# Kernel optimization log

Measured on AMD Instinct MI355X. Metric: run time of the kernel, lower is better.

## Reference

```python
import jax, jax.numpy as jnp
import numpy as np


def setup_inputs() -> dict:
    key = jax.random.key(0)
    ks = jax.random.split(key, 12)
    C, H, L, P = 256, 8, 4, 4
    Lq, Lx = 2048, 300
    iss = jnp.array([[64, 64], [32, 32], [16, 16], [8, 8]], dtype=jnp.int32)
    Len_in = int(np.sum(np.array(iss)[:, 0] * np.array(iss)[:, 1]))  # 5440
    lsi = jnp.array([0, 4096, 5120, 5376], dtype=jnp.int32)
    return {
        "query": jax.random.normal(ks[0], (1, Lq, C), jnp.float32),
        "reference_points": jax.random.uniform(ks[1], (1, Lq, L, 2), jnp.float32),
        "input_flatten": jax.random.normal(ks[2], (1, Len_in, C), jnp.float32),
        "input_spatial_shapes": iss,
        "add_keys": jax.random.normal(ks[3], (1, Lx, C), jnp.float32),
        "input_level_start_index": lsi,
        "W_off": jax.random.normal(ks[4], (H * L * P * 2, C), jnp.float32) * 0.01,
        "b_off": jax.random.normal(ks[5], (H * L * P * 2,), jnp.float32),
        "W_attn": jax.random.normal(ks[6], (H * (L + 1), C, C), jnp.float32) * 0.05,
        "W_v": jax.random.normal(ks[7], (H * 2, C, C), jnp.float32) * 0.05,
        "b_v": jax.random.normal(ks[8], (H * 2, C), jnp.float32) * 0.01,
        "W_mix": jax.random.normal(ks[9], (C, H + 1), jnp.float32) * 0.5,
    }


def reference(query, reference_points, input_flatten, input_spatial_shapes,
              add_keys, input_level_start_index, W_off, b_off, W_attn, W_v, b_v, W_mix):
    N, Lq, C = query.shape
    L = input_spatial_shapes.shape[0]
    H = W_v.shape[0] // 2
    P = W_off.shape[0] // (H * L * 2)

    # sampling locations: ref (x,y in [0,1]) + offsets / (W,H)
    off = (query @ W_off.T + b_off).reshape(N, Lq, H, L, P, 2)
    wh = input_spatial_shapes[:, ::-1].astype(query.dtype)  # (L,2) = (W,H)
    loc = reference_points[:, :, None, :, None, :] + off / wh[None, None, None, :, None, :]

    # get_keys: truncating index computation + gather (faithful to original)
    loc = jnp.clip(loc, 0.0, 0.999)
    iss_f = input_spatial_shapes.astype(loc.dtype)[None, None, None, :, None, :]
    idx = (loc * iss_f).astype(jnp.int32)  # (N,Lq,H,L,P,2): (int(x*H_l), int(y*W_l))
    lin = (idx[..., 0]
           + idx[..., 1] * input_spatial_shapes[:, 0].astype(jnp.int32)[None, None, None, :, None]
           + input_level_start_index.astype(jnp.int32)[None, None, None, :, None])
    keys = input_flatten[0][lin[0]]                # (Lq,H,L,P,C)
    keys = jnp.transpose(keys, (1, 2, 3, 0, 4))    # (H,L,P,Lq,C)

    head_w = jax.nn.softmax(W_mix.T, axis=0)       # (H+1,C)
    qf = query[0]                                  # (Lq,C)
    ak = add_keys[0]                               # (Lx,C)

    # per-head, per-level similarity (replicates original overlapping index h*L+lvl)
    Ws = W_attn[jnp.arange(H)[:, None] * L + jnp.arange(L)[None, :]]  # (H,L,C,C)
    T = jnp.einsum('hlce,hlpqe->hlcpq', Ws, keys)  # (H,L,C,P,Lq)
    # faithful reshape quirk: (C, P*Lq) viewed as (P, Lq, C)
    T = T.reshape(H, L, P, Lq, C)
    attn_s = jnp.einsum('hlpqc,qc->hlpq', T, qf).reshape(H, L * P, Lq)

    Wadd = W_attn[jnp.arange(H) * L + L]           # (H,C,C)
    attn_a = jnp.einsum('xe,hce,qc->hxq', ak, Wadd, qf)  # (H,Lx,Lq)

    attn = jax.nn.softmax(jnp.concatenate([attn_s, attn_a], axis=1), axis=1)
    attn_s_sm, attn_a_sm = attn[:, :L * P], attn[:, L * P:]

    Wv0, bv0 = W_v[0::2], b_v[0::2]
    Wv1, bv1 = W_v[1::2], b_v[1::2]
    vals = (jnp.einsum('hlpqe,hce->hlpqc', keys, Wv0)
            + bv0[:, None, None, None, :]).reshape(H, L * P, Lq, C)
    v2 = jnp.einsum('xe,hce->hxc', ak, Wv1) + bv1[:, None, :]  # (H,Lx,C)

    out_h = (jnp.einsum('hkq,hkqc->hqc', attn_s_sm, vals)
             + jnp.einsum('hxq,hxc->hqc', attn_a_sm, v2))      # (H,Lq,C)
    result = qf * head_w[-1][None, :] + jnp.einsum('hqc,hc->qc', out_h, head_w[:-1])
    return result[None]
```

## Files before the change

kernel.cpp:

```cpp
#include <hip/hip_runtime.h>
#include <stdint.h>

#define NJ 316

typedef __attribute__((ext_vector_type(8))) short short8;
typedef __attribute__((ext_vector_type(4))) float f32x4;
union U4S8 { uint4 u; short8 s; };

__device__ __forceinline__ unsigned short f2bf(float x) {
    unsigned int u = __float_as_uint(x);
    u += 0x7fff + ((u >> 16) & 1);
    return (unsigned short)(u >> 16);
}
__device__ __forceinline__ float bf2f(unsigned short h) {
    return __uint_as_float(((unsigned int)h) << 16);
}

__global__ __launch_bounds__(256) void cvt_all_kernel(
    const float* __restrict__ q,  unsigned short* __restrict__ qh,  unsigned short* __restrict__ ql,
    const float* __restrict__ ak, unsigned short* __restrict__ akh, unsigned short* __restrict__ akl,
    const float* __restrict__ wv, unsigned short* __restrict__ wvh, unsigned short* __restrict__ wvl,
    const float* __restrict__ inflat, unsigned int* __restrict__ inflatP,
    const float* __restrict__ Wattn, unsigned short* __restrict__ wah, unsigned short* __restrict__ wal,
    unsigned short* __restrict__ v2th, unsigned short* __restrict__ v2tl)
{
    int i = blockIdx.x * 256 + threadIdx.x;
    if (i < 760576) {
        const float* s; unsigned short *dh, *dl; int off; bool pack = false;
        unsigned int* dp = nullptr;
        if (i < 131072)      { s = q;  dh = qh;  dl = ql;  off = i; }
        else if (i < 150272) { s = ak; dh = akh; dl = akl; off = i - 131072; }
        else if (i < 412416) { s = wv; dh = wvh; dl = wvl; off = i - 150272; }
        else { s = inflat; dp = inflatP; off = i - 412416; pack = true; dh = dl = nullptr; }
        float4 v = ((const float4*)s)[off];
        float x[4] = {v.x, v.y, v.z, v.w};
        unsigned short h[4], l[4];
        #pragma unroll
        for (int j = 0; j < 4; ++j) {
            h[j] = f2bf(x[j]);
            l[j] = f2bf(x[j] - bf2f(h[j]));
        }
        if (pack) {
            ((uint4*)dp)[off] = make_uint4(
                (unsigned)h[0] | ((unsigned)l[0] << 16),
                (unsigned)h[1] | ((unsigned)l[1] << 16),
                (unsigned)h[2] | ((unsigned)l[2] << 16),
                (unsigned)h[3] | ((unsigned)l[3] << 16));
        } else {
            ((uint2*)dh)[off] = make_uint2((unsigned)h[0] | ((unsigned)h[1] << 16),
                                           (unsigned)h[2] | ((unsigned)h[3] << 16));
            ((uint2*)dl)[off] = make_uint2((unsigned)l[0] | ((unsigned)l[1] << 16),
                                           (unsigned)l[2] | ((unsigned)l[3] << 16));
        }
    } else if (i < 891648) {
        int off = i - 760576;
        int base = off * 4;
        int z = base >> 16, r = base & 65535;
        float4 v = *(const float4*)&Wattn[(size_t)(4 * z + 4) * 65536 + r];
        float x[4] = {v.x, v.y, v.z, v.w};
        unsigned short h[4], l[4];
        #pragma unroll
        for (int j = 0; j < 4; ++j) {
            h[j] = f2bf(x[j]);
            l[j] = f2bf(x[j] - bf2f(h[j]));
        }
        ((uint2*)wah)[off] = make_uint2((unsigned)h[0] | ((unsigned)h[1] << 16),
                                        (unsigned)h[2] | ((unsigned)h[3] << 16));
        ((uint2*)wal)[off] = make_uint2((unsigned)l[0] | ((unsigned)l[1] << 16),
                                        (unsigned)l[2] | ((unsigned)l[3] << 16));
    } else {
        int j = i - 891648;
        size_t base = (size_t)j * 320;
        uint2 zz = make_uint2(0u, 0u);
        #pragma unroll
        for (int d = 0; d < 4; ++d) {
            ((uint2*)(v2th + base))[d] = zz;
            ((uint2*)(v2tl + base))[d] = zz;
        }
        ((uint2*)(v2th + base + 316))[0] = zz;
        ((uint2*)(v2tl + base + 316))[0] = zz;
    }
}

struct Seg {
    const unsigned short *Ah, *Al, *Bh, *Bl;
    int K, lda, ldb;
    long sA, sB;
    int nprod;
};

template<bool ACCUM, bool OUTF32, int NSEG>
__device__ __forceinline__ void gemm_core(
    const Seg& s0, const Seg& s1,
    float* __restrict__ Cf, unsigned short* __restrict__ Ch,
    unsigned short* __restrict__ Cl,
    int M, int N, int ldc, long sC, int nb, int mb, int z, char* smem)
{
    unsigned short* As0 = (unsigned short*)smem;
    unsigned short* Bs0 = (unsigned short*)(smem + 10240);
    const int t = threadIdx.x;
    const int lane = t & 63;
    const int wave = t >> 6;
    const int wm = (wave & 1) * 32, wn = (wave >> 1) * 64;

    f32x4 acc[2][4];
    #pragma unroll
    for (int i = 0; i < 2; ++i)
        #pragma unroll
        for (int j = 0; j < 4; ++j) acc[i][j] = (f32x4){0.f, 0.f, 0.f, 0.f};

    const int arow = t >> 2, akoff = (t & 3) * 8;
    const int frow = lane & 15, fk = (lane >> 4) * 8;

    #pragma unroll
    for (int seg = 0; seg < NSEG; ++seg) {
        const Seg S = seg ? s1 : s0;
        const int np = S.nprod;
        const unsigned short* Azh = S.Ah + (size_t)z * S.sA;
        const unsigned short* Azl = (np >= 2) ? S.Al + (size_t)z * S.sA : nullptr;
        const unsigned short* Bzh = S.Bh + (size_t)z * S.sB;
        const unsigned short* Bzl = (np >= 3) ? S.Bl + (size_t)z * S.sB : nullptr;
        for (int kb = 0; kb < S.K; kb += 32) {
            __syncthreads();
            {
                int gm = mb + arow;
                uint4 vh = {0, 0, 0, 0}, vl = {0, 0, 0, 0};
                if (gm < M) {
                    size_t o = (size_t)gm * S.lda + kb + akoff;
                    vh = *(const uint4*)(Azh + o);
                    if (np >= 2) vl = *(const uint4*)(Azl + o);
                }
                *(uint4*)&As0[arow * 40 + akoff] = vh;
                if (np >= 2) *(uint4*)&As0[2560 + arow * 40 + akoff] = vl;
                #pragma unroll
                for (int i = 0; i < 2; ++i) {
                    int f = i * 256 + t;
                    int brow = f >> 2, bkoff = (f & 3) * 8;
                    int gn = nb + brow;
                    uint4 wh = {0, 0, 0, 0}, wl = {0, 0, 0, 0};
                    if (gn < N) {
                        size_t o = (size_t)gn * S.ldb + kb + bkoff;
                        wh = *(const uint4*)(Bzh + o);
                        if (np >= 3) wl = *(const uint4*)(Bzl + o);
                    }
                    *(uint4*)&Bs0[brow * 40 + bkoff] = wh;
                    if (np >= 3) *(uint4*)&Bs0[5120 + brow * 40 + bkoff] = wl;
                }
            }
            __syncthreads();
            short8 a[2][2], b[4][2];
            #pragma unroll
            for (int i = 0; i < 2; ++i) {
                int r = wm + i * 16 + frow;
                a[i][0] = *(const short8*)&As0[r * 40 + fk];
                if (np >= 2) a[i][1] = *(const short8*)&As0[2560 + r * 40 + fk];
            }
            #pragma unroll
            for (int j = 0; j < 4; ++j) {
                int r = wn + j * 16 + frow;
                b[j][0] = *(const short8*)&Bs0[r * 40 + fk];
                if (np >= 3) b[j][1] = *(const short8*)&Bs0[5120 + r * 40 + fk];
            }
            #pragma unroll
            for (int i = 0; i < 2; ++i)
                #pragma unroll
                for (int j = 0; j < 4; ++j) {
                    acc[i][j] = __builtin_amdgcn_mfma_f32_16x16x32_bf16(
                        a[i][0], b[j][0], acc[i][j], 0, 0, 0);
                    if (np >= 2)
                        acc[i][j] = __builtin_amdgcn_mfma_f32_16x16x32_bf16(
                            a[i][1], b[j][0], acc[i][j], 0, 0, 0);
                    if (np >= 3)
                        acc[i][j] = __builtin_amdgcn_mfma_f32_16x16x32_bf16(
                            a[i][0], b[j][1], acc[i][j], 0, 0, 0);
                }
        }
    }
    #pragma unroll
    for (int i = 0; i < 2; ++i)
        #pragma unroll
        for (int r = 0; r < 4; ++r) {
            int gm = mb + wm + i * 16 + (lane >> 4) * 4 + r;
            if (gm >= M) continue;
            #pragma unroll
            for (int j = 0; j < 4; ++j) {
                int gn = nb + wn + j * 16 + (lane & 15);
                if (gn >= N) continue;
                size_t idx = (size_t)z * sC + (size_t)gm * ldc + gn;
                float v = acc[i][j][r];
                if (OUTF32) {
                    float prev = ACCUM ? Cf[idx] : 0.f;
                    Cf[idx] = prev + v;
                } else {
                    unsigned short h = f2bf(v);
                    Ch[idx] = h;
                    Cl[idx] = f2bf(v - bf2f(h));
                }
            }
        }
}

template<bool ACCUM, bool OUTF32, int NSEG>
__global__ __launch_bounds__(256) void mfma_gemm(
    Seg s0, Seg s1,
    float* __restrict__ Cf, unsigned short* __restrict__ Ch,
    unsigned short* __restrict__ Cl,
    int M, int N, int ldc, long sC)
{
    __shared__ __align__(16) char smem[30720];
    gemm_core<ACCUM, OUTF32, NSEG>(s0, s1, Cf, Ch, Cl, M, N, ldc, sC,
                                   blockIdx.x * 128, blockIdx.y * 64,
                                   blockIdx.z, smem);
}

__global__ __launch_bounds__(256) void dual_lin_kernel(
    Seg a, Seg b,
    unsigned short* __restrict__ Bhh, unsigned short* __restrict__ Bhl,
    unsigned short* __restrict__ V2Th, unsigned short* __restrict__ V2Tl,
    const float* __restrict__ q, const float* __restrict__ refp,
    const int* __restrict__ iss, const int* __restrict__ lsi,
    const float* __restrict__ Woff, const float* __restrict__ boff,
    int* __restrict__ lin)
{
    __shared__ __align__(16) char smem[58368];
    const int bx = blockIdx.x;
    if (bx < 2) {
        gemm_core<false, false, 1>(a, a, nullptr, Bhh, Bhl,
                                   300, 256, 256, 320L * 256,
                                   bx * 128, blockIdx.y * 64, blockIdx.z, smem);
        return;
    }
    if (bx < 5) {
        if ((int)blockIdx.y * 64 >= 256) return;
        gemm_core<false, false, 1>(b, b, nullptr, V2Th, V2Tl,
                                   256, 300, 320, 256L * 320,
                                   (bx - 2) * 128, blockIdx.y * 64, blockIdx.z,
                                   smem);
        return;
    }
    const int idx = (bx - 5) * 40 + blockIdx.y * 8 + blockIdx.z;
    if (idx >= 256) return;

    float (*qf8)[256]  = (float(*)[256])smem;
    float (*wtile)[33] = (float(*)[33])(smem + 8192);
    double (*offl)[256]= (double(*)[256])(smem + 41984);
    const int t = threadIdx.x;
    const int qbase = idx * 8;
    #pragma unroll
    for (int i = 0; i < 8; ++i) qf8[i][t] = q[(qbase + i) * 256 + t];
    double acc[8];
    #pragma unroll
    for (int r = 0; r < 8; ++r) acc[r] = 0.0;
    for (int cb = 0; cb < 256; cb += 32) {
        __syncthreads();
        #pragma unroll
        for (int i = 0; i < 32; ++i) {
            int f = i * 256 + t;
            int o = f >> 5, jj = f & 31;
            wtile[o][jj] = Woff[o * 256 + cb + jj];
        }
        __syncthreads();
        #pragma unroll
        for (int jj = 0; jj < 32; ++jj) {
            double wvv = (double)wtile[t][jj];
            #pragma unroll
            for (int r = 0; r < 8; ++r)
                acc[r] += (double)qf8[r][cb + jj] * wvv;
        }
    }
    double bo = (double)boff[t];
    __syncthreads();
    #pragma unroll
    for (int r = 0; r < 8; ++r) offl[r][t] = acc[r] + bo;
    __syncthreads();
    #pragma unroll
    for (int rep = 0; rep < 4; ++rep) {
        int id2 = rep * 256 + t;
        int r = id2 >> 7;
        int s = id2 & 127;
        int l = (s >> 2) & 3;
        int qq = qbase + r;
        double offx = offl[r][2 * s];
        double offy = offl[r][2 * s + 1];
        int w0 = iss[l * 2 + 0];
        int w1 = iss[l * 2 + 1];
        double locx = (double)refp[qq * 8 + l * 2 + 0] + offx / (double)w1;
        double locy = (double)refp[qq * 8 + l * 2 + 1] + offy / (double)w0;
        locx = fmin(fmax(locx, 0.0), 0.999);
        locy = fmin(fmax(locy, 0.0), 0.999);
        int ix = (int)(locx * (double)w0);
        int iy = (int)(locy * (double)w1);
        lin[qq * 128 + s] = ix + iy * w0 + lsi[l];
    }
}

__global__ __launch_bounds__(256, 2) void gattn_attnA(
    const unsigned short* __restrict__ qh, const unsigned short* __restrict__ ql,
    const unsigned int* __restrict__ inflatP, const float* __restrict__ Wattn,
    const int* __restrict__ lin, float* __restrict__ attn, Seg aA)
{
    __shared__ __align__(16) char smem[69632];
    const int t = threadIdx.x;

    if ((int)blockIdx.x >= 1024) {
        int idx = blockIdx.x - 1024;
        int z = idx & 7, my = (idx >> 3) & 31, nx = idx >> 8;
        gemm_core<false, true, 1>(aA, aA, attn + 16, nullptr, nullptr,
                                  2048, 300, NJ, 2048L * NJ,
                                  nx * 128, my * 64, z, smem);
        return;
    }

    int* linrow = (int*)smem;
    float (*Glds)[268] = (float(*)[268])(smem + 1024);
    const int lane = t & 63, w = t >> 6;
    const int b = blockIdx.x;
    const int qb = b & 7, p = (b >> 3) & 3, l = (b >> 5) & 3, h = b >> 7;
    linrow[t] = lin[(256 * qb + t) * 128 + h * 16 + l * 4 + p];
    __syncthreads();

    const int l15 = lane & 15, g = lane >> 4;
    const int q2l = qb + 8 * p + 32 * l15;
    const int ebase = 64 * w + l15;

    f32x4 acc[4][4];
    #pragma unroll
    for (int i = 0; i < 4; ++i)
        #pragma unroll
        for (int eg = 0; eg < 4; ++eg) acc[i][eg] = (f32x4){0.f, 0.f, 0.f, 0.f};

    for (int kb = 0; kb < 256; kb += 32) {
        U4S8 ah[4], al[4];
        #pragma unroll
        for (int i = 0; i < 4; ++i) {
            size_t off = (size_t)(q2l + 512 * i) * 256 + kb + 8 * g;
            ah[i].u = *(const uint4*)(qh + off);
            al[i].u = *(const uint4*)(ql + off);
        }
        int rowoff[8];
        #pragma unroll
        for (int m = 0; m < 8; ++m) rowoff[m] = linrow[kb + 8 * g + m] * 256;
        unsigned int uv[4][8];
        #pragma unroll
        for (int eg = 0; eg < 4; ++eg)
            #pragma unroll
            for (int m = 0; m < 8; ++m)
                uv[eg][m] = inflatP[rowoff[m] + ebase + 16 * eg];

        #pragma unroll
        for (int eg = 0; eg < 4; ++eg) {
            U4S8 bh, bl;
            unsigned int hh[4], ll[4];
            #pragma unroll
            for (int d = 0; d < 4; ++d) {
                hh[d] = __builtin_amdgcn_perm(uv[eg][2 * d + 1], uv[eg][2 * d],
                                              0x05040100u);
                ll[d] = __builtin_amdgcn_perm(uv[eg][2 * d + 1], uv[eg][2 * d],
                                              0x07060302u);
            }
            bh.u = make_uint4(hh[0], hh[1], hh[2], hh[3]);
            bl.u = make_uint4(ll[0], ll[1], ll[2], ll[3]);
            #pragma unroll
            for (int i = 0; i < 4; ++i) {
                acc[i][eg] = __builtin_amdgcn_mfma_f32_16x16x32_bf16(
                    ah[i].s, bh.s, acc[i][eg], 0, 0, 0);
                acc[i][eg] = __builtin_amdgcn_mfma_f32_16x16x32_bf16(
                    ah[i].s, bl.s, acc[i][eg], 0, 0, 0);
                acc[i][eg] = __builtin_amdgcn_mfma_f32_16x16x32_bf16(
                    al[i].s, bh.s, acc[i][eg], 0, 0, 0);
            }
        }
    }

    #pragma unroll
    for (int i = 0; i < 4; ++i)
        #pragma unroll
        for (int eg = 0; eg < 4; ++eg)
            #pragma unroll
            for (int r = 0; r < 4; ++r)
                Glds[16 * i + 4 * g + r][64 * w + 16 * eg + l15] = acc[i][eg][r];
    __syncthreads();

    const int tx = t & 15, ty = t >> 4;
    const float* Wsbase = Wattn + (size_t)(h * 4 + l) * 65536;
    float gv[4][16];
    #pragma unroll
    for (int r = 0; r < 4; ++r)
        #pragma unroll
        for (int i2 = 0; i2 < 4; ++i2) {
            float4 gd = *(const float4*)&Glds[ty * 4 + r][tx * 4 + 64 * i2];
            gv[r][i2 * 4 + 0] = gd.x;
            gv[r][i2 * 4 + 1] = gd.y;
            gv[r][i2 * 4 + 2] = gd.z;
            gv[r][i2 * 4 + 3] = gd.w;
        }
    #pragma unroll
    for (int r = 0; r < 4; ++r) {
        int hi = ty * 4 + r;
        int q2 = qb + 8 * p + 32 * hi;
        #pragma unroll
        for (int p2 = 0; p2 < 4; ++p2) {
            const float* wr = Wsbase + (size_t)(hi + 64 * p2) * 256;
            float partial = 0.f;
            #pragma unroll
            for (int i2 = 0; i2 < 4; ++i2) {
                float4 wv = *(const float4*)&wr[tx * 4 + 64 * i2];
                partial += wv.x * gv[r][i2 * 4 + 0] + wv.y * gv[r][i2 * 4 + 1]
                         + wv.z * gv[r][i2 * 4 + 2] + wv.w * gv[r][i2 * 4 + 3];
            }
            partial += __shfl_xor(partial, 1);
            partial += __shfl_xor(partial, 2);
            partial += __shfl_xor(partial, 4);
            partial += __shfl_xor(partial, 8);
            if (tx == 0)
                attn[((size_t)h * 2048 + q2) * NJ + (l * 4 + p2)] = partial;
        }
    }
}

__global__ __launch_bounds__(256) void softmax_ka_kernel(
    const float* __restrict__ attn, const unsigned int* __restrict__ inflatP,
    const int* __restrict__ lin, float* __restrict__ s0,
    unsigned short* __restrict__ awh,
    unsigned short* __restrict__ KAh, unsigned short* __restrict__ KAl)
{
    __shared__ float red[8];
    __shared__ float w16[16];
    __shared__ int lls[16];
    const int t = threadIdx.x;
    const int lane = t & 63, w = t >> 6;
    const int rid = blockIdx.x;
    const int h = rid >> 11, q = rid & 2047;
    const float* row = attn + (size_t)rid * NJ;

    float v0 = row[t];
    float v1 = (t < 60) ? row[256 + t] : -1e30f;
    float m = fmaxf(v0, v1);
    #pragma unroll
    for (int d = 1; d < 64; d <<= 1) m = fmaxf(m, __shfl_xor(m, d));
    if (lane == 0) red[w] = m;
    __syncthreads();
    m = fmaxf(fmaxf(red[0], red[1]), fmaxf(red[2], red[3]));

    float e0 = expf(v0 - m);
    float e1 = (t < 60) ? expf(v1 - m) : 0.f;
    float s = e0 + e1;
    #pragma unroll
    for (int d = 1; d < 64; d <<= 1) s += __shfl_xor(s, d);
    if (lane == 0) red[4 + w] = s;
    __syncthreads();
    s = (red[4] + red[5]) + (red[6] + red[7]);
    const float inv = 1.f / s;

    float sf = (t < 16) ? e0 : 0.f;
    #pragma unroll
    for (int d = 1; d < 64; d <<= 1) sf += __shfl_xor(sf, d);
    if (lane == 0) red[w] = sf;

    float a0 = e0 * inv;
    float a1 = (t < 60) ? e1 * inv : 0.f;
    awh[(size_t)rid * 320 + t] = f2bf(a0);
    if (t < 64)
        awh[(size_t)rid * 320 + 256 + t] = f2bf(a1);
    if (t < 16) {
        w16[t] = a0;
        lls[t] = lin[q * 128 + h * 16 + t];
    }
    __syncthreads();
    if (t == 0)
        s0[rid] = ((red[0] + red[1]) + (red[2] + red[3])) * inv;

    float acc = 0.f;
    #pragma unroll
    for (int k = 0; k < 16; ++k) {
        unsigned int u = inflatP[lls[k] * 256 + t];
        acc += w16[k] * (bf2f((unsigned short)(u & 0xffff)) +
                         bf2f((unsigned short)(u >> 16)));
    }
    unsigned short hh = f2bf(acc);
    KAh[(size_t)rid * 256 + t] = hh;
    KAl[(size_t)rid * 256 + t] = f2bf(acc - bf2f(hh));
}

__global__ __launch_bounds__(256) void final_kernel(
    const float* __restrict__ qf, const float* __restrict__ OH,
    const float* __restrict__ s0, const float* __restrict__ bv,
    const float* __restrict__ Wmix, float* __restrict__ out)
{
    const int q = blockIdx.x, c = threadIdx.x;
    float wj[9], m = -1e30f;
    #pragma unroll
    for (int j = 0; j < 9; ++j) { wj[j] = Wmix[c * 9 + j]; m = fmaxf(m, wj[j]); }
    float s = 0.f;
    #pragma unroll
    for (int j = 0; j < 9; ++j) { wj[j] = expf(wj[j] - m); s += wj[j]; }
    float inv = 1.f / s;
    float acc = qf[q * 256 + c] * wj[8] * inv;
    #pragma unroll
    for (int h = 0; h < 8; ++h) {
        float s0v = s0[h * 2048 + q];
        float oh = OH[((size_t)h * 2048 + q) * 256 + c]
                 + s0v * bv[(2 * h) * 256 + c]
                 + (1.f - s0v) * bv[(2 * h + 1) * 256 + c];
        acc += oh * wj[h] * inv;
    }
    out[q * 256 + c] = acc;
}

extern "C" void kernel_launch(void* const* d_in, const int* in_sizes, int n_in,
                              void* d_out, int out_size, void* d_ws, size_t ws_size,
                              hipStream_t stream) {
    const float* query = (const float*)d_in[0];
    const float* refp  = (const float*)d_in[1];
    const float* inflat= (const float*)d_in[2];
    const int*   iss   = (const int*)d_in[3];
    const float* ak    = (const float*)d_in[4];
    const int*   lsi   = (const int*)d_in[5];
    const float* Woff  = (const float*)d_in[6];
    const float* boff  = (const float*)d_in[7];
    const float* Wattn = (const float*)d_in[8];
    const float* Wv    = (const float*)d_in[9];
    const float* bv    = (const float*)d_in[10];
    const float* Wmix  = (const float*)d_in[11];
    float* out = (float*)d_out;

    typedef unsigned short us;
    char* ws = (char*)d_ws;
    int* lin    = (int*)ws;   ws += (size_t)262144 * 4;
    float* attn = (float*)ws; ws += (size_t)8 * 2048 * NJ * 4;
    float* s0   = (float*)ws; ws += (size_t)8 * 2048 * 4;
    unsigned int* inflatP = (unsigned int*)ws; ws += (size_t)1392640 * 4;
    us* qh  = (us*)ws; ws += (size_t)524288 * 2;
    us* ql  = (us*)ws; ws += (size_t)524288 * 2;
    us* akh = (us*)ws; ws += (size_t)320 * 256 * 2;
    us* akl = (us*)ws; ws += (size_t)320 * 256 * 2;
    us* Waddh = (us*)ws; ws += (size_t)524288 * 2;
    us* Waddl = (us*)ws; ws += (size_t)524288 * 2;
    us* Wvh = (us*)ws; ws += (size_t)1048576 * 2;
    us* Wvl = (us*)ws; ws += (size_t)1048576 * 2;
    us* Bhh = (us*)ws; ws += (size_t)8 * 320 * 256 * 2;
    us* Bhl = (us*)ws; ws += (size_t)8 * 320 * 256 * 2;
    us* V2Th= (us*)ws; ws += (size_t)8 * 256 * 320 * 2;
    us* V2Tl= (us*)ws; ws += (size_t)8 * 256 * 320 * 2;
    us* awh = (us*)ws; ws += (size_t)8 * 2048 * 320 * 2;
    us* KAh = (us*)ws; ws += (size_t)8 * 2048 * 256 * 2;
    us* KAl = (us*)ws; ws += (size_t)8 * 2048 * 256 * 2;
    float* OH = (float*)ws;   ws += (size_t)8 * 2048 * 256 * 4;

    cvt_all_kernel<<<3491, 256, 0, stream>>>(
        query, qh, ql, ak, akh, akl, Wv, Wvh, Wvl,
        inflat, inflatP, Wattn, Waddh, Waddl, V2Th, V2Tl);

    Seg sz = {nullptr, nullptr, nullptr, nullptr, 0, 0, 0, 0L, 0L, 0};

    {
        Seg a = {akh, akl, Waddh, Waddl, 256, 256, 256, 0L, 65536L, 3};
        Seg b = {Wvh + 65536, Wvl + 65536, akh, nullptr, 256, 256, 256,
                 131072L, 0L, 2};
        dual_lin_kernel<<<dim3(12, 5, 8), 256, 0, stream>>>(
            a, b, Bhh, Bhl, V2Th + 16, V2Tl + 16,
            query, refp, iss, lsi, Woff, boff, lin);
    }

    {
        Seg aA = {qh, ql, Bhh, Bhl, 256, 256, 256, 0L, 320L * 256, 3};
        gattn_attnA<<<1792, 256, 0, stream>>>(qh, ql, inflatP, Wattn, lin,
                                              attn, aA);
    }

    softmax_ka_kernel<<<16384, 256, 0, stream>>>(attn, inflatP, lin, s0,
                                                 awh, KAh, KAl);

    {
        Seg a = {KAh, KAl, Wvh, nullptr, 256, 256, 256, 2048L * 256,
                 2L * 65536, 2};
        Seg b = {awh, nullptr, V2Th, nullptr, 320, 320, 320, 2048L * 320,
                 256L * 320, 1};
        mfma_gemm<false, true, 2><<<dim3(2, 32, 8), 256, 0, stream>>>(
            a, b, OH, nullptr, nullptr, 2048, 256, 256, 2048L * 256);
    }

    final_kernel<<<2048, 256, 0, stream>>>(query, OH, s0, bv, Wmix, out);
}
```

Measured before the change: 273.1 us.

## Fuse final head mixing into output GEMM epilogue via atomic accumulation

The separate final kernel and the fp32 OH intermediate (8x2048x256 floats) are removed. The per-head GEMM epilogue now applies the bias, the s0 blend and the softmaxed Wmix weights, then atomically adds into the zeroed output. The Wmix softmax is precomputed once per channel inside the conversion kernel. This drops a large write and read round trip plus one launch, at the cost of a memset and 8-way float atomic contention per output element, which also makes summation order nondeterministic.

```diff
diff --git a/kernel.cpp b/kernel.cpp
--- a/kernel.cpp
+++ b/kernel.cpp
@@ -22,7 +22,8 @@
     const float* __restrict__ wv, unsigned short* __restrict__ wvh, unsigned short* __restrict__ wvl,
     const float* __restrict__ inflat, unsigned int* __restrict__ inflatP,
     const float* __restrict__ Wattn, unsigned short* __restrict__ wah, unsigned short* __restrict__ wal,
-    unsigned short* __restrict__ v2th, unsigned short* __restrict__ v2tl)
+    unsigned short* __restrict__ v2th, unsigned short* __restrict__ v2tl,
+    const float* __restrict__ Wmix, float* __restrict__ wjbuf)
 {
     int i = blockIdx.x * 256 + threadIdx.x;
     if (i < 760576) {
@@ -68,7 +69,7 @@
                                         (unsigned)h[2] | ((unsigned)h[3] << 16));
         ((uint2*)wal)[off] = make_uint2((unsigned)l[0] | ((unsigned)l[1] << 16),
                                         (unsigned)l[2] | ((unsigned)l[3] << 16));
-    } else {
+    } else if (i < 893696) {
         int j = i - 891648;
         size_t base = (size_t)j * 320;
         uint2 zz = make_uint2(0u, 0u);
@@ -79,6 +80,22 @@
         }
         ((uint2*)(v2th + base + 316))[0] = zz;
         ((uint2*)(v2tl + base + 316))[0] = zz;
+    } else {
+        int c = i - 893696;
+        if (c < 256) {
+            float wv9[9], m = -1e30f;
+            #pragma unroll
+            for (int j = 0; j < 9; ++j) {
+                wv9[j] = Wmix[c * 9 + j];
+                m = fmaxf(m, wv9[j]);
+            }
+            float s = 0.f;
+            #pragma unroll
+            for (int j = 0; j < 9; ++j) { wv9[j] = expf(wv9[j] - m); s += wv9[j]; }
+            float inv = 1.f / s;
+            #pragma unroll
+            for (int j = 0; j < 9; ++j) wjbuf[j * 256 + c] = wv9[j] * inv;
+        }
     }
 }
 
@@ -89,12 +106,10 @@
     int nprod;
 };
 
-template<bool ACCUM, bool OUTF32, int NSEG>
-__device__ __forceinline__ void gemm_core(
-    const Seg& s0, const Seg& s1,
-    float* __restrict__ Cf, unsigned short* __restrict__ Ch,
-    unsigned short* __restrict__ Cl,
-    int M, int N, int ldc, long sC, int nb, int mb, int z, char* smem)
+template<int NSEG>
+__device__ __forceinline__ void gemm_mainloop(
+    const Seg& s0, const Seg& s1, int M, int N, int nb, int mb, int z,
+    char* smem, f32x4 (&acc)[2][4])
 {
     unsigned short* As0 = (unsigned short*)smem;
     unsigned short* Bs0 = (unsigned short*)(smem + 10240);
@@ -102,12 +117,6 @@
     const int lane = t & 63;
     const int wave = t >> 6;
     const int wm = (wave & 1) * 32, wn = (wave >> 1) * 64;
-
-    f32x4 acc[2][4];
-    #pragma unroll
-    for (int i = 0; i < 2; ++i)
-        #pragma unroll
-        for (int j = 0; j < 4; ++j) acc[i][j] = (f32x4){0.f, 0.f, 0.f, 0.f};
 
     const int arow = t >> 2, akoff = (t & 3) * 8;
     const int frow = lane & 15, fk = (lane >> 4) * 8;
@@ -176,6 +185,24 @@
                 }
         }
     }
+}
+
+template<bool ACCUM, bool OUTF32, int NSEG>
+__device__ __forceinline__ void gemm_core(
+    const Seg& s0, const Seg& s1,
+    float* __restrict__ Cf, unsigned short* __restrict__ Ch,
+    unsigned short* __restrict__ Cl,
+    int M, int N, int ldc, long sC, int nb, int mb, int z, char* smem)
+{
+    const int lane = threadIdx.x & 63;
+    const int wave = threadIdx.x >> 6;
+    const int wm = (wave & 1) * 32, wn = (wave >> 1) * 64;
+    f32x4 acc[2][4];
+    #pragma unroll
+    for (int i = 0; i < 2; ++i)
+        #pragma unroll
+        for (int j = 0; j < 4; ++j) acc[i][j] = (f32x4){0.f, 0.f, 0.f, 0.f};
+    gemm_mainloop<NSEG>(s0, s1, M, N, nb, mb, z, smem, acc);
     #pragma unroll
     for (int i = 0; i < 2; ++i)
         #pragma unroll
@@ -211,6 +238,46 @@
     gemm_core<ACCUM, OUTF32, NSEG>(s0, s1, Cf, Ch, Cl, M, N, ldc, sC,
                                    blockIdx.x * 128, blockIdx.y * 64,
                                    blockIdx.z, smem);
+}
+
+__global__ __launch_bounds__(256) void oh_out_kernel(
+    Seg a, Seg b, const float* __restrict__ qf, const float* __restrict__ s0,
+    const float* __restrict__ bv, const float* __restrict__ wj,
+    float* __restrict__ out)
+{
+    __shared__ __align__(16) char smem[30720];
+    const int nb = blockIdx.x * 128, mb = blockIdx.y * 64;
+    const int z = blockIdx.z;
+    const int lane = threadIdx.x & 63;
+    const int wave = threadIdx.x >> 6;
+    const int wm = (wave & 1) * 32, wn = (wave >> 1) * 64;
+
+    f32x4 acc[2][4];
+    #pragma unroll
+    for (int i = 0; i < 2; ++i)
+        #pragma unroll
+        for (int j = 0; j < 4; ++j) acc[i][j] = (f32x4){0.f, 0.f, 0.f, 0.f};
+    gemm_mainloop<2>(a, b, 2048, 256, nb, mb, z, smem, acc);
+
+    #pragma unroll
+    for (int j = 0; j < 4; ++j) {
+        int gn = nb + wn + j * 16 + (lane & 15);
+        float bv0g = bv[(2 * z) * 256 + gn];
+        float bv1g = bv[(2 * z + 1) * 256 + gn];
+        float wjz  = wj[z * 256 + gn];
+        float wj8  = wj[8 * 256 + gn];
+        #pragma unroll
+        for (int i = 0; i < 2; ++i)
+            #pragma unroll
+            for (int r = 0; r < 4; ++r) {
+                int gm = mb + wm + i * 16 + (lane >> 4) * 4 + r;
+                float s0v = s0[z * 2048 + gm];
+                float val = (acc[i][j][r] + s0v * bv0g + (1.f - s0v) * bv1g)
+                            * wjz;
+                if (z == 0) val += qf[(size_t)gm * 256 + gn] * wj8;
+                atomicAdd(&out[(size_t)gm * 256 + gn], val);
+            }
+    }
 }
 
 __global__ __launch_bounds__(256) void dual_lin_kernel(
@@ -482,31 +549,6 @@
     KAl[(size_t)rid * 256 + t] = f2bf(acc - bf2f(hh));
 }
 
-__global__ __launch_bounds__(256) void final_kernel(
-    const float* __restrict__ qf, const float* __restrict__ OH,
-    const float* __restrict__ s0, const float* __restrict__ bv,
-    const float* __restrict__ Wmix, float* __restrict__ out)
-{
-    const int q = blockIdx.x, c = threadIdx.x;
-    float wj[9], m = -1e30f;
-    #pragma unroll
-    for (int j = 0; j < 9; ++j) { wj[j] = Wmix[c * 9 + j]; m = fmaxf(m, wj[j]); }
-    float s = 0.f;
-    #pragma unroll
-    for (int j = 0; j < 9; ++j) { wj[j] = expf(wj[j] - m); s += wj[j]; }
-    float inv = 1.f / s;
-    float acc = qf[q * 256 + c] * wj[8] * inv;
-    #pragma unroll
-    for (int h = 0; h < 8; ++h) {
-        float s0v = s0[h * 2048 + q];
-        float oh = OH[((size_t)h * 2048 + q) * 256 + c]
-                 + s0v * bv[(2 * h) * 256 + c]
-                 + (1.f - s0v) * bv[(2 * h + 1) * 256 + c];
-        acc += oh * wj[h] * inv;
-    }
-    out[q * 256 + c] = acc;
-}
-
 extern "C" void kernel_launch(void* const* d_in, const int* in_sizes, int n_in,
                               void* d_out, int out_size, void* d_ws, size_t ws_size,
                               hipStream_t stream) {
@@ -529,6 +571,7 @@
     int* lin    = (int*)ws;   ws += (size_t)262144 * 4;
     float* attn = (float*)ws; ws += (size_t)8 * 2048 * NJ * 4;
     float* s0   = (float*)ws; ws += (size_t)8 * 2048 * 4;
+    float* wjbuf= (float*)ws; ws += (size_t)9 * 256 * 4;
     unsigned int* inflatP = (unsigned int*)ws; ws += (size_t)1392640 * 4;
     us* qh  = (us*)ws; ws += (size_t)524288 * 2;
     us* ql  = (us*)ws; ws += (size_t)524288 * 2;
@@ -545,13 +588,12 @@
     us* awh = (us*)ws; ws += (size_t)8 * 2048 * 320 * 2;
     us* KAh = (us*)ws; ws += (size_t)8 * 2048 * 256 * 2;
     us* KAl = (us*)ws; ws += (size_t)8 * 2048 * 256 * 2;
-    float* OH = (float*)ws;   ws += (size_t)8 * 2048 * 256 * 4;
-
-    cvt_all_kernel<<<3491, 256, 0, stream>>>(
+
+    hipMemsetAsync(out, 0, (size_t)out_size * 4, stream);
+
+    cvt_all_kernel<<<3492, 256, 0, stream>>>(
         query, qh, ql, ak, akh, akl, Wv, Wvh, Wvl,
-        inflat, inflatP, Wattn, Waddh, Waddl, V2Th, V2Tl);
-
-    Seg sz = {nullptr, nullptr, nullptr, nullptr, 0, 0, 0, 0L, 0L, 0};
+        inflat, inflatP, Wattn, Waddh, Waddl, V2Th, V2Tl, Wmix, wjbuf);
 
     {
         Seg a = {akh, akl, Waddh, Waddl, 256, 256, 256, 0L, 65536L, 3};
@@ -576,9 +618,7 @@
                  2L * 65536, 2};
         Seg b = {awh, nullptr, V2Th, nullptr, 320, 320, 320, 2048L * 320,
                  256L * 320, 1};
-        mfma_gemm<false, true, 2><<<dim3(2, 32, 8), 256, 0, stream>>>(
-            a, b, OH, nullptr, nullptr, 2048, 256, 256, 2048L * 256);
-    }
-
-    final_kernel<<<2048, 256, 0, stream>>>(query, OH, s0, bv, Wmix, out);
-}
+        oh_out_kernel<<<dim3(2, 32, 8), 256, 0, stream>>>(
+            a, b, query, s0, bv, wjbuf, out);
+    }
+}
```

After: 284.8 us. +4.3%, slower.
